# Kernel optimization log

Measured on AMD Instinct MI355X. Metric: run time of the kernel, lower is better.

## Reference

```python
import jax, jax.numpy as jnp
import numpy as np

PAD = 1  # padding from init_kwargs

def setup_inputs() -> dict:
    key = jax.random.key(0)
    k1, k2 = jax.random.split(key)
    x = jax.random.normal(k1, (1, 256, 224, 224), dtype=jnp.float32)
    # Conv2d_mvm weight: [out_channels, in_channels, kh, kw]
    weight = jax.random.normal(k2, (256, 256, 3, 3), dtype=jnp.float32) * 0.05
    return {"x": x, "weight": weight}

def reference(x, weight):
    # Exact math of the bit-sliced crossbar conv forward: stride-1 cross-correlation
    # with zero padding, no bias, output squeezed to [C_out, H_out, W_out]
    # (the original forward emits no batch dimension).
    out = jax.lax.conv_general_dilated(
        x, weight,
        window_strides=(1, 1),
        padding=((PAD, PAD), (PAD, PAD)),
        dimension_numbers=("NCHW", "OIHW", "NCHW"),
    )
    return out[0]  # [C_out, H_out, W_out]
```

## Files before the change

kernel.cpp:

```cpp
#include <hip/hip_runtime.h>


#define H 224
#define W 224
#define NPOS (H*W)
#define CI 256
#define CO 256
#define KDIM 2304
#define HP 226
#define XP_ELEMS (HP*HP*CI)
#define AP_ELEMS (CO*KDIM)

typedef __bf16 bf16x8 __attribute__((ext_vector_type(8)));
typedef float f32x4 __attribute__((ext_vector_type(4)));
typedef unsigned short u16x4 __attribute__((ext_vector_type(4)));
typedef unsigned short u16x8 __attribute__((ext_vector_type(8)));

__device__ __forceinline__ unsigned short f2bf(float f) {
    unsigned int u = __float_as_uint(f);
    u += 0x7fff + ((u >> 16) & 1);
    return (unsigned short)(u >> 16);
}

__device__ __forceinline__ void load_lds16(const unsigned short* g, unsigned short* l) {
    __builtin_amdgcn_global_load_lds(
        (const __attribute__((address_space(1))) void*)g,
        (__attribute__((address_space(3))) void*)l,
        16, 0, 0);
}

#define XT_BLOCKS 3136
#define WT_BLOCKS 256
#define BORDER_V8 28800
#define ROW_V8 7232
__global__ void prep_kernel(const float* __restrict__ x, const float* __restrict__ w,
                            unsigned short* __restrict__ ap, unsigned short* __restrict__ xp) {
    __shared__ unsigned short smem[64 * 68];
    const int bx = blockIdx.x;
    const int t = threadIdx.x;

    if (bx < XT_BLOCKS) {
        const unsigned int pBase = (unsigned int)(bx % 784) * 64;
        const unsigned int ciBase = (unsigned int)(bx / 784) * 64;
        {
            const int p4 = (t & 15) * 4;
            const int c0 = t >> 4;
#pragma unroll
            for (int i = 0; i < 4; ++i) {
                const int ci_l = c0 + i * 16;
                const f32x4 v = *(const f32x4*)&x[(ciBase + ci_l) * NPOS + pBase + p4];
                u16x4 s;
                s[0] = f2bf(v[0]); s[1] = f2bf(v[1]); s[2] = f2bf(v[2]); s[3] = f2bf(v[3]);
                *(u16x4*)&smem[ci_l * 68 + p4] = s;
            }
        }
        __syncthreads();
        {
            const int ci0 = (t & 7) * 8;
            const int pr = t >> 3;
#pragma unroll
            for (int j = 0; j < 2; ++j) {
                const int p_l = pr + j * 32;
                const unsigned int p = pBase + p_l;
                const unsigned int hi = p / W, wi = p - hi * W;
                u16x8 v;
#pragma unroll
                for (int k = 0; k < 8; ++k) v[k] = smem[(ci0 + k) * 68 + p_l];
                *(u16x8*)&xp[((hi + 1) * HP + (wi + 1)) * CI + ciBase + ci0] = v;
            }
        }
    } else if (bx < XT_BLOCKS + WT_BLOCKS) {
        const int co = bx - XT_BLOCKS;
        const float* wc = w + co * KDIM;
#pragma unroll
        for (int i = 0; i < 9; ++i)
            smem[i * 256 + t] = f2bf(wc[i * 256 + t]);
        __syncthreads();
        unsigned short* apc = ap + co * KDIM;
#pragma unroll
        for (int tap = 0; tap < 9; ++tap)
            apc[tap * 256 + t] = smem[t * 9 + tap];
    } else {
        const int idx = (bx - XT_BLOCKS - WT_BLOCKS) * 256 + t;
        if (idx < BORDER_V8) {
            unsigned short* p;
            if (idx < 2 * ROW_V8) {
                const int r = idx / ROW_V8;
                const int off = idx - r * ROW_V8;
                p = xp + r * (225 * HP * CI) + off * 8;
            } else {
                const int i2 = idx - 2 * ROW_V8;
                const int seg = i2 >> 5;
                const int o = i2 & 31;
                const int hp = 1 + (seg >> 1);
                const int wp = (seg & 1) * 225;
                p = xp + (hp * HP + wp) * CI + o * 8;
            }
            *(u16x8*)p = (u16x8){0, 0, 0, 0, 0, 0, 0, 0};
        }
    }
}

__global__ __launch_bounds__(512, 1) void gemm_conv_kernel(
    const unsigned short* __restrict__ Ap,
    const unsigned short* __restrict__ Xp,
    float* __restrict__ out)
{
    __shared__ unsigned short Als[3][8192];
    __shared__ unsigned short Bls[3][8192];

    const int tid = threadIdx.x;
    const int Nb = blockIdx.x;
    const int wave = tid >> 6;
    const int wm = wave >> 2;
    const int wn = wave & 3;
    const int lane = tid & 63;
    const int ln15 = lane & 15;
    const int quad = lane >> 4;
    const int xsw = ((quad ^ (ln15 & 3)) * 8);

    const int rl = lane >> 2;
    const int sc = (lane & 3) ^ (rl & 3);

    const unsigned short* a_src[2];
    const unsigned short* b_src[2];
#pragma unroll
    for (int j = 0; j < 2; ++j) {
        const int row = j * 128 + wave * 16 + rl;
        a_src[j] = Ap + row * KDIM + sc * 8;
        unsigned int p = Nb * 256 + row;
        unsigned int hi = p / W, wi = p - hi * W;
        b_src[j] = Xp + (hi * HP + wi) * CI + sc * 8;
    }

    f32x4 acc[8][4];
#pragma unroll
    for (int mi = 0; mi < 8; ++mi)
#pragma unroll
        for (int ni = 0; ni < 4; ++ni)
            acc[mi][ni] = (f32x4){0.f, 0.f, 0.f, 0.f};

    auto stageA = [&](int kt, int buf) {
        const int aoff = kt * 32;
#pragma unroll
        for (int j = 0; j < 2; ++j)
            load_lds16(a_src[j] + aoff, &Als[buf][(j * 8 + wave) * 512]);
    };
    auto stageB = [&](int kt, int buf) {
        const int tap = kt >> 3;
        const int dh = tap / 3, dw = tap - dh * 3;
        const int boff = (dh * HP + dw) * CI + (kt & 7) * 32;
#pragma unroll
        for (int j = 0; j < 2; ++j)
            load_lds16(b_src[j] + boff, &Bls[buf][(j * 8 + wave) * 512]);
    };

    bf16x8 af[4], bfr[4];
    const int aBase = (wm * 128 + ln15) * 32 + xsw;
    const int bBase = (wn * 64 + ln15) * 32 + xsw;

    auto ldA = [&](int c, int half) {
#pragma unroll
        for (int mi = 0; mi < 4; ++mi)
            af[mi] = *(const bf16x8*)&Als[c][aBase + (half * 64 + mi * 16) * 32];
    };
    auto ldB = [&](int c) {
#pragma unroll
        for (int ni = 0; ni < 4; ++ni)
            bfr[ni] = *(const bf16x8*)&Bls[c][bBase + ni * 16 * 32];
    };
    auto mfma16 = [&](int half) {
        __builtin_amdgcn_s_setprio(1);
#pragma unroll
        for (int mi = 0; mi < 4; ++mi)
#pragma unroll
            for (int ni = 0; ni < 4; ++ni)
                acc[half * 4 + mi][ni] = __builtin_amdgcn_mfma_f32_16x16x32_bf16(
                    af[mi], bfr[ni], acc[half * 4 + mi][ni], 0, 0, 0);
        __builtin_amdgcn_s_setprio(0);
    };

    stageA(0, 0); stageB(0, 0);
    stageA(1, 1); stageB(1, 1);
    asm volatile("s_waitcnt vmcnt(4)" ::: "memory");
    __builtin_amdgcn_s_barrier();

    int c = 0;
    for (int kt = 0; kt < 70; ++kt) {
        const int s = (c == 0) ? 2 : c - 1;
        ldA(c, 0); ldB(c);
        stageA(kt + 2, s);
        __builtin_amdgcn_s_barrier();
        asm volatile("s_waitcnt lgkmcnt(0)" ::: "memory");
        __builtin_amdgcn_sched_barrier(0);
        mfma16(0);
        __builtin_amdgcn_s_barrier();
        ldA(c, 1);
        stageB(kt + 2, s);
        asm volatile("s_waitcnt vmcnt(4)" ::: "memory");
        __builtin_amdgcn_s_barrier();
        asm volatile("s_waitcnt lgkmcnt(0)" ::: "memory");
        __builtin_amdgcn_sched_barrier(0);
        mfma16(1);
        __builtin_amdgcn_s_barrier();
        c = (c == 2) ? 0 : c + 1;
    }
    {
        ldA(c, 0); ldB(c);
        __builtin_amdgcn_s_barrier();
        asm volatile("s_waitcnt lgkmcnt(0)" ::: "memory");
        __builtin_amdgcn_sched_barrier(0);
        mfma16(0);
        __builtin_amdgcn_s_barrier();
        ldA(c, 1);
        asm volatile("s_waitcnt vmcnt(0)" ::: "memory");
        __builtin_amdgcn_s_barrier();
        asm volatile("s_waitcnt lgkmcnt(0)" ::: "memory");
        __builtin_amdgcn_sched_barrier(0);
        mfma16(1);
        __builtin_amdgcn_s_barrier();
        c = (c == 2) ? 0 : c + 1;
    }
    {
        ldA(c, 0); ldB(c);
        asm volatile("s_waitcnt lgkmcnt(0)" ::: "memory");
        __builtin_amdgcn_sched_barrier(0);
        mfma16(0);
        ldA(c, 1);
        asm volatile("s_waitcnt lgkmcnt(0)" ::: "memory");
        __builtin_amdgcn_sched_barrier(0);
        mfma16(1);
    }

    const int pcol = Nb * 256 + wn * 64 + ln15;
    const int corow = wm * 128 + quad * 4;
#pragma unroll
    for (int mi = 0; mi < 8; ++mi)
#pragma unroll
        for (int ni = 0; ni < 4; ++ni)
#pragma unroll
            for (int r = 0; r < 4; ++r)
                out[(corow + mi * 16 + r) * NPOS + pcol + ni * 16] = acc[mi][ni][r];
}

extern "C" void kernel_launch(void* const* d_in, const int* in_sizes, int n_in,
                              void* d_out, int out_size, void* d_ws, size_t ws_size,
                              hipStream_t stream) {
    const float* x = (const float*)d_in[0];
    const float* w = (const float*)d_in[1];
    float* out = (float*)d_out;

    unsigned short* xp = (unsigned short*)d_ws;
    unsigned short* ap = xp + XP_ELEMS;

    prep_kernel<<<XT_BLOCKS + WT_BLOCKS + 113, 256, 0, stream>>>(x, w, ap, xp);
    gemm_conv_kernel<<<dim3(NPOS / 256), 512, 0, stream>>>(ap, xp, out);
}
```

Before: 187.2 us.

## Restructure GEMM pipeline to double-buffered BK=64 stages in unified LDS

After: 164.3 us. 1.14x faster.

```diff
diff --git a/kernel.cpp b/kernel.cpp
--- a/kernel.cpp
+++ b/kernel.cpp
@@ -101,13 +101,33 @@
     }
 }
 
+
+#define READ_A(base, half)                                                      \
+    _Pragma("unroll")                                                           \
+    for (int mi = 0; mi < 4; ++mi)                                              \
+        af[mi] = *(const bf16x8*)&lds[(base) + arow + ((half) * 4 + mi) * 512];
+
+#define READ_B(base)                                                            \
+    _Pragma("unroll")                                                           \
+    for (int ni = 0; ni < 4; ++ni)                                              \
+        bf[ni] = *(const bf16x8*)&lds[(base) + brow + ni * 512];
+
+#define MFMA16(half)                                                            \
+    __builtin_amdgcn_s_setprio(1);                                              \
+    _Pragma("unroll")                                                           \
+    for (int mi = 0; mi < 4; ++mi)                                              \
+        _Pragma("unroll")                                                       \
+        for (int ni = 0; ni < 4; ++ni)                                          \
+            acc[(half) * 4 + mi][ni] = __builtin_amdgcn_mfma_f32_16x16x32_bf16( \
+                af[mi], bf[ni], acc[(half) * 4 + mi][ni], 0, 0, 0);             \
+    __builtin_amdgcn_s_setprio(0);
+
 __global__ __launch_bounds__(512, 1) void gemm_conv_kernel(
     const unsigned short* __restrict__ Ap,
     const unsigned short* __restrict__ Xp,
     float* __restrict__ out)
 {
-    __shared__ unsigned short Als[3][8192];
-    __shared__ unsigned short Bls[3][8192];
+    __shared__ unsigned short lds[65536];
 
     const int tid = threadIdx.x;
     const int Nb = blockIdx.x;
@@ -117,20 +137,20 @@
     const int lane = tid & 63;
     const int ln15 = lane & 15;
     const int quad = lane >> 4;
-    const int xsw = ((quad ^ (ln15 & 3)) * 8);
-
-    const int rl = lane >> 2;
-    const int sc = (lane & 3) ^ (rl & 3);
-
+    const int slot8 = (quad ^ (ln15 & 3)) * 8;
+    const int arow = (wm * 128 + ln15) * 32 + slot8;
+    const int brow = 32768 + (wn * 64 + ln15) * 32 + slot8;
+
+    const int c4 = (tid & 3) ^ ((tid >> 2) & 3);
     const unsigned short* a_src[2];
     const unsigned short* b_src[2];
 #pragma unroll
     for (int j = 0; j < 2; ++j) {
-        const int row = j * 128 + wave * 16 + rl;
-        a_src[j] = Ap + row * KDIM + sc * 8;
-        unsigned int p = Nb * 256 + row;
+        const int r = j * 128 + (tid >> 2);
+        a_src[j] = Ap + r * KDIM + c4 * 8;
+        unsigned int p = Nb * 256 + r;
         unsigned int hi = p / W, wi = p - hi * W;
-        b_src[j] = Xp + (hi * HP + wi) * CI + sc * 8;
+        b_src[j] = Xp + (hi * HP + wi) * CI + c4 * 8;
     }
 
     f32x4 acc[8][4];
@@ -140,96 +160,71 @@
         for (int ni = 0; ni < 4; ++ni)
             acc[mi][ni] = (f32x4){0.f, 0.f, 0.f, 0.f};
 
-    auto stageA = [&](int kt, int buf) {
-        const int aoff = kt * 32;
+    auto stageA = [&](int kt, int k) {
+        const int dst = ((kt & 1) * 2 + k) * 8192;
+        const int off = kt * 64 + k * 32;
 #pragma unroll
         for (int j = 0; j < 2; ++j)
-            load_lds16(a_src[j] + aoff, &Als[buf][(j * 8 + wave) * 512]);
+            load_lds16(a_src[j] + off, &lds[dst + (j * 8 + wave) * 512]);
     };
-    auto stageB = [&](int kt, int buf) {
-        const int tap = kt >> 3;
-        const int dh = tap / 3, dw = tap - dh * 3;
-        const int boff = (dh * HP + dw) * CI + (kt & 7) * 32;
+    auto stageB = [&](int kt, int k) {
+        const int dst = 32768 + ((kt & 1) * 2 + k) * 8192;
+        const int tap = kt >> 2;
+        const int dh = (tap * 11) >> 5;
+        const int dw = tap - dh * 3;
+        const int off = (dh * HP + dw) * CI + (kt & 3) * 64 + k * 32;
 #pragma unroll
         for (int j = 0; j < 2; ++j)
-            load_lds16(b_src[j] + boff, &Bls[buf][(j * 8 + wave) * 512]);
+            load_lds16(b_src[j] + off, &lds[dst + (j * 8 + wave) * 512]);
     };
 
-    bf16x8 af[4], bfr[4];
-    const int aBase = (wm * 128 + ln15) * 32 + xsw;
-    const int bBase = (wn * 64 + ln15) * 32 + xsw;
-
-    auto ldA = [&](int c, int half) {
-#pragma unroll
-        for (int mi = 0; mi < 4; ++mi)
-            af[mi] = *(const bf16x8*)&Als[c][aBase + (half * 64 + mi * 16) * 32];
-    };
-    auto ldB = [&](int c) {
-#pragma unroll
-        for (int ni = 0; ni < 4; ++ni)
-            bfr[ni] = *(const bf16x8*)&Bls[c][bBase + ni * 16 * 32];
-    };
-    auto mfma16 = [&](int half) {
-        __builtin_amdgcn_s_setprio(1);
-#pragma unroll
-        for (int mi = 0; mi < 4; ++mi)
-#pragma unroll
-            for (int ni = 0; ni < 4; ++ni)
-                acc[half * 4 + mi][ni] = __builtin_amdgcn_mfma_f32_16x16x32_bf16(
-                    af[mi], bfr[ni], acc[half * 4 + mi][ni], 0, 0, 0);
-        __builtin_amdgcn_s_setprio(0);
-    };
-
-    stageA(0, 0); stageB(0, 0);
-    stageA(1, 1); stageB(1, 1);
+    bf16x8 af[4], bf[4];
+
+    stageA(0, 0); stageB(0, 0); stageA(0, 1); stageB(0, 1);
     asm volatile("s_waitcnt vmcnt(4)" ::: "memory");
     __builtin_amdgcn_s_barrier();
 
-    int c = 0;
-    for (int kt = 0; kt < 70; ++kt) {
-        const int s = (c == 0) ? 2 : c - 1;
-        ldA(c, 0); ldB(c);
-        stageA(kt + 2, s);
-        __builtin_amdgcn_s_barrier();
-        asm volatile("s_waitcnt lgkmcnt(0)" ::: "memory");
-        __builtin_amdgcn_sched_barrier(0);
-        mfma16(0);
-        __builtin_amdgcn_s_barrier();
-        ldA(c, 1);
-        stageB(kt + 2, s);
-        asm volatile("s_waitcnt vmcnt(4)" ::: "memory");
-        __builtin_amdgcn_s_barrier();
-        asm volatile("s_waitcnt lgkmcnt(0)" ::: "memory");
-        __builtin_amdgcn_sched_barrier(0);
-        mfma16(1);
-        __builtin_amdgcn_s_barrier();
-        c = (c == 2) ? 0 : c + 1;
-    }
-    {
-        ldA(c, 0); ldB(c);
-        __builtin_amdgcn_s_barrier();
-        asm volatile("s_waitcnt lgkmcnt(0)" ::: "memory");
-        __builtin_amdgcn_sched_barrier(0);
-        mfma16(0);
-        __builtin_amdgcn_s_barrier();
-        ldA(c, 1);
-        asm volatile("s_waitcnt vmcnt(0)" ::: "memory");
-        __builtin_amdgcn_s_barrier();
-        asm volatile("s_waitcnt lgkmcnt(0)" ::: "memory");
-        __builtin_amdgcn_sched_barrier(0);
-        mfma16(1);
-        __builtin_amdgcn_s_barrier();
-        c = (c == 2) ? 0 : c + 1;
-    }
-    {
-        ldA(c, 0); ldB(c);
-        asm volatile("s_waitcnt lgkmcnt(0)" ::: "memory");
-        __builtin_amdgcn_sched_barrier(0);
-        mfma16(0);
-        ldA(c, 1);
-        asm volatile("s_waitcnt lgkmcnt(0)" ::: "memory");
-        __builtin_amdgcn_sched_barrier(0);
-        mfma16(1);
+    for (int kt = 0; kt < 36; ++kt) {
+        const int pi = (kt & 1) * 2;
+        const int b0 = pi * 8192;
+        const int b1 = (pi + 1) * 8192;
+        const bool st = kt < 35;
+        READ_A(b0, 0) READ_B(b0)
+        if (st) stageA(kt + 1, 0);
+        __builtin_amdgcn_s_barrier();
+        asm volatile("s_waitcnt lgkmcnt(0)" ::: "memory");
+        __builtin_amdgcn_sched_barrier(0);
+        MFMA16(0)
+        __builtin_amdgcn_s_barrier();
+        READ_A(b0, 1)
+        if (st) {
+            stageB(kt + 1, 0);
+            asm volatile("s_waitcnt vmcnt(4)" ::: "memory");
+        } else {
+            asm volatile("s_waitcnt vmcnt(0)" ::: "memory");
+        }
+        __builtin_amdgcn_s_barrier();
+        asm volatile("s_waitcnt lgkmcnt(0)" ::: "memory");
+        __builtin_amdgcn_sched_barrier(0);
+        MFMA16(1)
+        __builtin_amdgcn_s_barrier();
+        READ_A(b1, 0) READ_B(b1)
+        if (st) stageA(kt + 1, 1);
+        __builtin_amdgcn_s_barrier();
+        asm volatile("s_waitcnt lgkmcnt(0)" ::: "memory");
+        __builtin_amdgcn_sched_barrier(0);
+        MFMA16(0)
+        __builtin_amdgcn_s_barrier();
+        READ_A(b1, 1)
+        if (st) {
+            stageB(kt + 1, 1);
+            asm volatile("s_waitcnt vmcnt(4)" ::: "memory");
+        }
+        __builtin_amdgcn_s_barrier();
+        asm volatile("s_waitcnt lgkmcnt(0)" ::: "memory");
+        __builtin_amdgcn_sched_barrier(0);
+        MFMA16(1)
+        __builtin_amdgcn_s_barrier();
     }
 
     const int pcol = Nb * 256 + wn * 64 + ln15;
```
